# Performance work log

Measured on AMD Instinct MI355X. Metric: run time of the kernel, lower is better.

## Reference

```python
import jax, jax.numpy as jnp
import numpy as np

B, N, H = 4, 512, 64


def setup_inputs() -> dict:
    key = jax.random.key(0)
    ks = jax.random.split(key, 20)
    s = 0.05
    inp = {
        "positions": jax.random.uniform(ks[0], (B, N, 2), dtype=jnp.float32) * 10.0,
        "box_size": 10,
        # encoder: Linear(2,H) -> ReLU -> Linear(H,H)
        "enc_w1": jax.random.normal(ks[1], (2, H), jnp.float32) * s,
        "enc_b1": jnp.zeros((H,), jnp.float32),
        "enc_w2": jax.random.normal(ks[2], (H, H), jnp.float32) * s,
        "enc_b2": jnp.zeros((H,), jnp.float32),
        # message: Linear(2H+1,H) -> ReLU -> Linear(H,H)
        "msg_w1": jax.random.normal(ks[3], (2 * H + 1, H), jnp.float32) * s,
        "msg_b1": jnp.zeros((H,), jnp.float32),
        "msg_w2": jax.random.normal(ks[4], (H, H), jnp.float32) * s,
        "msg_b2": jnp.zeros((H,), jnp.float32),
        # update: Linear(2H,H) -> ReLU -> Linear(H,H)
        "upd_w1": jax.random.normal(ks[5], (2 * H, H), jnp.float32) * s,
        "upd_b1": jnp.zeros((H,), jnp.float32),
        "upd_w2": jax.random.normal(ks[6], (H, H), jnp.float32) * s,
        "upd_b2": jnp.zeros((H,), jnp.float32),
        # decoder: Linear(H,H) -> ReLU -> Linear(H,2)
        "dec_w1": jax.random.normal(ks[7], (H, H), jnp.float32) * s,
        "dec_b1": jnp.zeros((H,), jnp.float32),
        "dec_w2": jax.random.normal(ks[8], (H, 2), jnp.float32) * s,
        "dec_b2": jnp.zeros((2,), jnp.float32),
    }
    return inp


def reference(positions, box_size, enc_w1, enc_b1, enc_w2, enc_b2,
              msg_w1, msg_b1, msg_w2, msg_b2,
              upd_w1, upd_b1, upd_w2, upd_b2,
              dec_w1, dec_b1, dec_w2, dec_b2):
    box = jnp.float32(box_size)
    n = positions.shape[1]

    # encoder
    h = jax.nn.relu(positions @ enc_w1 + enc_b1) @ enc_w2 + enc_b2  # (B,N,H)

    # pairwise PBC displacement: r[b,i,j] = pos_j - pos_i (minimum image)
    r = positions[:, None, :, :] - positions[:, :, None, :]  # (B,N,N,2)
    r = r - box * jnp.round(r / box)
    dist = jnp.linalg.norm(r, axis=-1, keepdims=True)  # (B,N,N,1)

    # message MLP layer 1 without materializing concat: split msg_w1 rows
    w_i, w_j, w_d = msg_w1[:h.shape[-1]], msg_w1[h.shape[-1]:2 * h.shape[-1]], msg_w1[2 * h.shape[-1]:]
    a_i = h @ w_i  # (B,N,H) depends only on receiver i
    a_j = h @ w_j  # (B,N,H) depends only on sender j
    pre = a_i[:, :, None, :] + a_j[:, None, :, :] + dist * w_d[0] + msg_b1  # (B,N,N,H)
    m = jax.nn.relu(pre) @ msg_w2 + msg_b2  # (B,N,N,H)

    # mean over j != i
    mask = (1.0 - jnp.eye(n, dtype=m.dtype))[None, :, :, None]
    agg = jnp.sum(m * mask, axis=2) / jnp.float32(n - 1)  # (B,N,H)

    u_in = jnp.concatenate([h, agg], axis=-1)  # (B,N,2H)
    u = jax.nn.relu(u_in @ upd_w1 + upd_b1) @ upd_w2 + upd_b2
    forces = jax.nn.relu(u @ dec_w1 + dec_b1) @ dec_w2 + dec_b2  # (B,N,2)
    return forces
```

## Files before the change

kernel.cpp:

```cpp
#include <hip/hip_runtime.h>

#define BB 4
#define NN 512
#define HH 64
#define NODES (BB*NN)
#define SPLIT 8
#define JCH (NN/SPLIT)
#define TI 4

typedef float v4f __attribute__((ext_vector_type(4)));

__global__ __launch_bounds__(64) void enc_kernel(
    const float* __restrict__ pos,
    const float* __restrict__ enc_w1, const float* __restrict__ enc_b1,
    const float* __restrict__ enc_w2, const float* __restrict__ enc_b2,
    const float* __restrict__ msg_w1,
    float* __restrict__ h_out, float* __restrict__ ai_out, float* __restrict__ aj_out)
{
    const int node = blockIdx.x;
    const int k = threadIdx.x;
    __shared__ float t_s[HH];
    __shared__ float h_s[HH];

    const float px = pos[node*2+0];
    const float py = pos[node*2+1];

    float t = fmaf(px, enc_w1[k], fmaf(py, enc_w1[HH + k], enc_b1[k]));
    t_s[k] = fmaxf(t, 0.f);
    __syncthreads();

    float h = enc_b2[k];
    #pragma unroll
    for (int m = 0; m < HH; ++m) h = fmaf(t_s[m], enc_w2[m*HH + k], h);
    h_s[k] = h;
    h_out[node*HH + k] = h;
    __syncthreads();

    float ai = 0.f, aj = 0.f;
    #pragma unroll
    for (int m = 0; m < HH; ++m) {
        const float hm = h_s[m];
        ai = fmaf(hm, msg_w1[m*HH + k],        ai);
        aj = fmaf(hm, msg_w1[(HH + m)*HH + k], aj);
    }
    ai_out[node*HH + k] = ai;
    aj_out[node*HH + k] = aj;
}

__global__ __launch_bounds__(256) void pair_kernel(
    const float* __restrict__ pos, const int* __restrict__ box_ptr,
    const float* __restrict__ msg_w1, const float* __restrict__ msg_b1,
    const float* __restrict__ ai, const float* __restrict__ aj,
    float* __restrict__ acc_part)
{
    const int w  = threadIdx.x >> 6;
    const int l  = threadIdx.x & 63;
    const int jgrp = l >> 4;
    const int kq   = l & 15;
    const int wj = blockIdx.x*4 + w;
    const int s  = wj & (SPLIT-1);
    const int ig = wj >> 3;
    const int b  = ig >> 7;
    const int i0 = (ig & 127) * TI;
    const int jch0 = s * JCH;

    const float box  = (float)box_ptr[0];
    const float hbox = 0.5f * box;

    __shared__ float dbuf[4][TI*64];
    float* db = dbuf[w];

    const float2* pos2 = (const float2*)pos;

    const v4f wd4 = *(const v4f*)(msg_w1 + 2*HH*HH + 4*kq);
    const v4f b1  = *(const v4f*)(msg_b1 + 4*kq);
    v4f base4[TI];
    float2 pi[TI];
    #pragma unroll
    for (int ii = 0; ii < TI; ++ii) {
        const int node = b*NN + i0 + ii;
        base4[ii] = *(const v4f*)(ai + (size_t)node*HH + 4*kq) + b1;
        pi[ii] = pos2[node];
    }

    {
        const float2 pj = pos2[b*NN + jch0 + l];
        #pragma unroll
        for (int ii = 0; ii < TI; ++ii) {
            float dx = pj.x - pi[ii].x;
            float dy = pj.y - pi[ii].y;
            dx -= (dx >  hbox) ? box : 0.f;
            dx += (dx < -hbox) ? box : 0.f;
            dy -= (dy >  hbox) ? box : 0.f;
            dy += (dy < -hbox) ? box : 0.f;
            db[ii*64 + (l&3)*16 + (l>>2)] = sqrtf(fmaf(dx, dx, dy*dy));
        }
    }
    __builtin_amdgcn_wave_barrier();

    v4f acc[TI];
    #pragma unroll
    for (int ii = 0; ii < TI; ++ii) acc[ii] = (v4f){0.f,0.f,0.f,0.f};

    #pragma unroll
    for (int t4 = 0; t4 < 4; ++t4) {
        v4f d4[TI];
        #pragma unroll
        for (int ii = 0; ii < TI; ++ii)
            d4[ii] = *(const v4f*)(db + ii*64 + jgrp*16 + 4*t4);
        #pragma unroll
        for (int u = 0; u < 4; ++u) {
            const int o = (t4*4 + u)*4 + jgrp;
            const v4f a4 = *(const v4f*)(aj + (size_t)(b*NN + jch0 + o)*HH + 4*kq);
            #pragma unroll
            for (int ii = 0; ii < TI; ++ii) {
                const float d = d4[ii][u];
                v4f t = __builtin_elementwise_fma((v4f)(d), wd4, a4 + base4[ii]);
                acc[ii] += __builtin_elementwise_max(t, (v4f){0.f,0.f,0.f,0.f});
            }
        }
    }

    #pragma unroll
    for (int ii = 0; ii < TI; ++ii) {
        #pragma unroll
        for (int c = 0; c < 4; ++c) {
            float v = acc[ii][c];
            v += __shfl_xor(v, 16, 64);
            v += __shfl_xor(v, 32, 64);
            acc[ii][c] = v;
        }
    }

    {
        const int ii = jgrp;
        const int i  = i0 + ii;
        v4f a = acc[ii];
        if ((i >> 6) == s) {
            const v4f ajs = *(const v4f*)(aj + (size_t)(b*NN + i)*HH + 4*kq);
            v4f t = base4[ii] + ajs;
            a -= __builtin_elementwise_max(t, (v4f){0.f,0.f,0.f,0.f});
        }
        *(v4f*)(acc_part + ((size_t)s*NODES + b*NN + i)*HH + 4*kq) = a;
    }
}

__global__ __launch_bounds__(64) void out_kernel(
    const float* __restrict__ h_in, const float* __restrict__ acc_in,
    const float* __restrict__ msg_w2, const float* __restrict__ msg_b2,
    const float* __restrict__ upd_w1, const float* __restrict__ upd_b1,
    const float* __restrict__ upd_w2, const float* __restrict__ upd_b2,
    const float* __restrict__ dec_w1, const float* __restrict__ dec_b1,
    const float* __restrict__ dec_w2, const float* __restrict__ dec_b2,
    float* __restrict__ out)
{
    const int node = blockIdx.x;
    const int k = threadIdx.x;
    __shared__ float acc_s[HH], h_s[HH], agg_s[HH], p_s[HH], u_s[HH];

    float a = 0.f;
    #pragma unroll
    for (int sl = 0; sl < SPLIT; ++sl)
        a += acc_in[((size_t)sl*NODES + node)*HH + k];
    acc_s[k] = a;
    h_s[k]   = h_in[node*HH + k];
    __syncthreads();

    const float inv = 1.f / (float)(NN - 1);
    float agg = 0.f;
    #pragma unroll
    for (int m = 0; m < HH; ++m) agg = fmaf(acc_s[m], msg_w2[m*HH + k], agg);
    agg = fmaf(agg, inv, msg_b2[k]);
    agg_s[k] = agg;
    __syncthreads();

    float p = upd_b1[k];
    #pragma unroll
    for (int m = 0; m < HH; ++m) p = fmaf(h_s[m],   upd_w1[m*HH + k],        p);
    #pragma unroll
    for (int m = 0; m < HH; ++m) p = fmaf(agg_s[m], upd_w1[(HH + m)*HH + k], p);
    p_s[k] = fmaxf(p, 0.f);
    __syncthreads();

    float u = upd_b2[k];
    #pragma unroll
    for (int m = 0; m < HH; ++m) u = fmaf(p_s[m], upd_w2[m*HH + k], u);
    u_s[k] = u;
    __syncthreads();

    float d1 = dec_b1[k];
    #pragma unroll
    for (int m = 0; m < HH; ++m) d1 = fmaf(u_s[m], dec_w1[m*HH + k], d1);
    d1 = fmaxf(d1, 0.f);

    float f0 = d1 * dec_w2[k*2 + 0];
    float f1 = d1 * dec_w2[k*2 + 1];
    #pragma unroll
    for (int off = 32; off >= 1; off >>= 1) {
        f0 += __shfl_xor(f0, off, 64);
        f1 += __shfl_xor(f1, off, 64);
    }
    if (k == 0) {
        out[node*2 + 0] = f0 + dec_b2[0];
        out[node*2 + 1] = f1 + dec_b2[1];
    }
}

extern "C" void kernel_launch(void* const* d_in, const int* in_sizes, int n_in,
                              void* d_out, int out_size, void* d_ws, size_t ws_size,
                              hipStream_t stream) {
    const float* pos    = (const float*)d_in[0];
    const int*   boxp   = (const int*)  d_in[1];
    const float* enc_w1 = (const float*)d_in[2];
    const float* enc_b1 = (const float*)d_in[3];
    const float* enc_w2 = (const float*)d_in[4];
    const float* enc_b2 = (const float*)d_in[5];
    const float* msg_w1 = (const float*)d_in[6];
    const float* msg_b1 = (const float*)d_in[7];
    const float* msg_w2 = (const float*)d_in[8];
    const float* msg_b2 = (const float*)d_in[9];
    const float* upd_w1 = (const float*)d_in[10];
    const float* upd_b1 = (const float*)d_in[11];
    const float* upd_w2 = (const float*)d_in[12];
    const float* upd_b2 = (const float*)d_in[13];
    const float* dec_w1 = (const float*)d_in[14];
    const float* dec_b1 = (const float*)d_in[15];
    const float* dec_w2 = (const float*)d_in[16];
    const float* dec_b2 = (const float*)d_in[17];

    float* ws   = (float*)d_ws;
    float* h    = ws;
    float* ai   = ws + (size_t)NODES*HH;
    float* aj   = ws + (size_t)2*NODES*HH;
    float* accp = ws + (size_t)3*NODES*HH;

    enc_kernel<<<NODES, 64, 0, stream>>>(pos, enc_w1, enc_b1, enc_w2, enc_b2,
                                         msg_w1, h, ai, aj);
    pair_kernel<<<(NODES/TI)*SPLIT/4, 256, 0, stream>>>(pos, boxp, msg_w1, msg_b1,
                                                        ai, aj, accp);
    out_kernel<<<NODES, 64, 0, stream>>>(h, accp, msg_w2, msg_b2,
                                         upd_w1, upd_b1, upd_w2, upd_b2,
                                         dec_w1, dec_b1, dec_w2, dec_b2,
                                         (float*)d_out);
}
```

Baseline: 29.74 us.

## Fuse pair aggregation with node MLP epilogue and batch encoder nodes per block

The pair kernel and the output MLP kernel are merged into one kernel. Each 512-thread block handles 4 receiver nodes, with its 8 waves covering the 8 j-slices, and reduces the partial sums through LDS instead of a global workspace. Wave 0 then runs the msg_w2/update/decoder MLP chain for those 4 nodes, sharing each weight row across them with shuffles and LDS. The encoder also processes 4 nodes per 256-thread block. This removes a kernel launch and the global round trip of partial accumulators. In exchange, the serial epilogue runs on a single wave while the other 7 waves exit.

```diff
diff --git a/kernel.cpp b/kernel.cpp
--- a/kernel.cpp
+++ b/kernel.cpp
@@ -4,149 +4,55 @@
 #define NN 512
 #define HH 64
 #define NODES (BB*NN)
-#define SPLIT 8
-#define JCH (NN/SPLIT)
+#define NSL 8
+#define JCH (NN/NSL)
 #define TI 4
 
 typedef float v4f __attribute__((ext_vector_type(4)));
 
-__global__ __launch_bounds__(64) void enc_kernel(
+__global__ __launch_bounds__(256) void enc_kernel(
     const float* __restrict__ pos,
     const float* __restrict__ enc_w1, const float* __restrict__ enc_b1,
     const float* __restrict__ enc_w2, const float* __restrict__ enc_b2,
     const float* __restrict__ msg_w1,
     float* __restrict__ h_out, float* __restrict__ ai_out, float* __restrict__ aj_out)
 {
-    const int node = blockIdx.x;
-    const int k = threadIdx.x;
-    __shared__ float t_s[HH];
-    __shared__ float h_s[HH];
+    const int w = threadIdx.x >> 6;
+    const int k = threadIdx.x & 63;
+    const int node = blockIdx.x*4 + w;
+    __shared__ float t_s[4][HH];
+    __shared__ float h_s[4][HH];
 
     const float px = pos[node*2+0];
     const float py = pos[node*2+1];
 
     float t = fmaf(px, enc_w1[k], fmaf(py, enc_w1[HH + k], enc_b1[k]));
-    t_s[k] = fmaxf(t, 0.f);
+    t_s[w][k] = fmaxf(t, 0.f);
     __syncthreads();
 
     float h = enc_b2[k];
     #pragma unroll
-    for (int m = 0; m < HH; ++m) h = fmaf(t_s[m], enc_w2[m*HH + k], h);
-    h_s[k] = h;
+    for (int m = 0; m < HH; ++m) h = fmaf(t_s[w][m], enc_w2[m*HH + k], h);
+    h_s[w][k] = h;
     h_out[node*HH + k] = h;
     __syncthreads();
 
-    float ai = 0.f, aj = 0.f;
+    float aiv = 0.f, ajv = 0.f;
     #pragma unroll
     for (int m = 0; m < HH; ++m) {
-        const float hm = h_s[m];
-        ai = fmaf(hm, msg_w1[m*HH + k],        ai);
-        aj = fmaf(hm, msg_w1[(HH + m)*HH + k], aj);
-    }
-    ai_out[node*HH + k] = ai;
-    aj_out[node*HH + k] = aj;
+        const float hm = h_s[w][m];
+        aiv = fmaf(hm, msg_w1[m*HH + k],        aiv);
+        ajv = fmaf(hm, msg_w1[(HH + m)*HH + k], ajv);
+    }
+    ai_out[node*HH + k] = aiv;
+    aj_out[node*HH + k] = ajv;
 }
 
-__global__ __launch_bounds__(256) void pair_kernel(
+__global__ __launch_bounds__(512, 4) void pairout_kernel(
     const float* __restrict__ pos, const int* __restrict__ box_ptr,
     const float* __restrict__ msg_w1, const float* __restrict__ msg_b1,
     const float* __restrict__ ai, const float* __restrict__ aj,
-    float* __restrict__ acc_part)
-{
-    const int w  = threadIdx.x >> 6;
-    const int l  = threadIdx.x & 63;
-    const int jgrp = l >> 4;
-    const int kq   = l & 15;
-    const int wj = blockIdx.x*4 + w;
-    const int s  = wj & (SPLIT-1);
-    const int ig = wj >> 3;
-    const int b  = ig >> 7;
-    const int i0 = (ig & 127) * TI;
-    const int jch0 = s * JCH;
-
-    const float box  = (float)box_ptr[0];
-    const float hbox = 0.5f * box;
-
-    __shared__ float dbuf[4][TI*64];
-    float* db = dbuf[w];
-
-    const float2* pos2 = (const float2*)pos;
-
-    const v4f wd4 = *(const v4f*)(msg_w1 + 2*HH*HH + 4*kq);
-    const v4f b1  = *(const v4f*)(msg_b1 + 4*kq);
-    v4f base4[TI];
-    float2 pi[TI];
-    #pragma unroll
-    for (int ii = 0; ii < TI; ++ii) {
-        const int node = b*NN + i0 + ii;
-        base4[ii] = *(const v4f*)(ai + (size_t)node*HH + 4*kq) + b1;
-        pi[ii] = pos2[node];
-    }
-
-    {
-        const float2 pj = pos2[b*NN + jch0 + l];
-        #pragma unroll
-        for (int ii = 0; ii < TI; ++ii) {
-            float dx = pj.x - pi[ii].x;
-            float dy = pj.y - pi[ii].y;
-            dx -= (dx >  hbox) ? box : 0.f;
-            dx += (dx < -hbox) ? box : 0.f;
-            dy -= (dy >  hbox) ? box : 0.f;
-            dy += (dy < -hbox) ? box : 0.f;
-            db[ii*64 + (l&3)*16 + (l>>2)] = sqrtf(fmaf(dx, dx, dy*dy));
-        }
-    }
-    __builtin_amdgcn_wave_barrier();
-
-    v4f acc[TI];
-    #pragma unroll
-    for (int ii = 0; ii < TI; ++ii) acc[ii] = (v4f){0.f,0.f,0.f,0.f};
-
-    #pragma unroll
-    for (int t4 = 0; t4 < 4; ++t4) {
-        v4f d4[TI];
-        #pragma unroll
-        for (int ii = 0; ii < TI; ++ii)
-            d4[ii] = *(const v4f*)(db + ii*64 + jgrp*16 + 4*t4);
-        #pragma unroll
-        for (int u = 0; u < 4; ++u) {
-            const int o = (t4*4 + u)*4 + jgrp;
-            const v4f a4 = *(const v4f*)(aj + (size_t)(b*NN + jch0 + o)*HH + 4*kq);
-            #pragma unroll
-            for (int ii = 0; ii < TI; ++ii) {
-                const float d = d4[ii][u];
-                v4f t = __builtin_elementwise_fma((v4f)(d), wd4, a4 + base4[ii]);
-                acc[ii] += __builtin_elementwise_max(t, (v4f){0.f,0.f,0.f,0.f});
-            }
-        }
-    }
-
-    #pragma unroll
-    for (int ii = 0; ii < TI; ++ii) {
-        #pragma unroll
-        for (int c = 0; c < 4; ++c) {
-            float v = acc[ii][c];
-            v += __shfl_xor(v, 16, 64);
-            v += __shfl_xor(v, 32, 64);
-            acc[ii][c] = v;
-        }
-    }
-
-    {
-        const int ii = jgrp;
-        const int i  = i0 + ii;
-        v4f a = acc[ii];
-        if ((i >> 6) == s) {
-            const v4f ajs = *(const v4f*)(aj + (size_t)(b*NN + i)*HH + 4*kq);
-            v4f t = base4[ii] + ajs;
-            a -= __builtin_elementwise_max(t, (v4f){0.f,0.f,0.f,0.f});
-        }
-        *(v4f*)(acc_part + ((size_t)s*NODES + b*NN + i)*HH + 4*kq) = a;
-    }
-}
-
-__global__ __launch_bounds__(64) void out_kernel(
-    const float* __restrict__ h_in, const float* __restrict__ acc_in,
+    const float* __restrict__ h_in,
     const float* __restrict__ msg_w2, const float* __restrict__ msg_b2,
     const float* __restrict__ upd_w1, const float* __restrict__ upd_b1,
     const float* __restrict__ upd_w2, const float* __restrict__ upd_b2,
@@ -154,55 +60,257 @@
     const float* __restrict__ dec_w2, const float* __restrict__ dec_b2,
     float* __restrict__ out)
 {
-    const int node = blockIdx.x;
-    const int k = threadIdx.x;
-    __shared__ float acc_s[HH], h_s[HH], agg_s[HH], p_s[HH], u_s[HH];
-
-    float a = 0.f;
+    const int w  = threadIdx.x >> 6;
+    const int l  = threadIdx.x & 63;
+    const int jgrp = l >> 4;
+    const int kq   = l & 15;
+    const int ig = blockIdx.x;
+    const int b  = ig >> 7;
+    const int i0 = (ig & 127) * TI;
+    const int node0 = b*NN + i0;
+    const int jch0  = w * JCH;
+
+    __shared__ float dbuf[NSL][TI*64];
+    __shared__ float acc_lds[NSL][TI][HH];
+    __shared__ float C1[TI][HH];
+    __shared__ float C2[TI][HH];
+
+    {
+        const float box  = (float)box_ptr[0];
+        const float hbox = 0.5f * box;
+        const float2* pos2 = (const float2*)pos;
+        float* db = dbuf[w];
+
+        const v4f wd4 = *(const v4f*)(msg_w1 + 2*HH*HH + 4*kq);
+        const v4f b1  = *(const v4f*)(msg_b1 + 4*kq);
+        v4f base4[TI];
+        float2 pi[TI];
+        #pragma unroll
+        for (int ii = 0; ii < TI; ++ii) {
+            base4[ii] = *(const v4f*)(ai + (size_t)(node0 + ii)*HH + 4*kq) + b1;
+            pi[ii] = pos2[node0 + ii];
+        }
+
+        {
+            const float2 pj = pos2[b*NN + jch0 + l];
+            #pragma unroll
+            for (int ii = 0; ii < TI; ++ii) {
+                float dx = pj.x - pi[ii].x;
+                float dy = pj.y - pi[ii].y;
+                dx -= (dx >  hbox) ? box : 0.f;
+                dx += (dx < -hbox) ? box : 0.f;
+                dy -= (dy >  hbox) ? box : 0.f;
+                dy += (dy < -hbox) ? box : 0.f;
+                db[ii*64 + (l&3)*16 + (l>>2)] = sqrtf(fmaf(dx, dx, dy*dy));
+            }
+        }
+        __builtin_amdgcn_wave_barrier();
+
+        v4f acc[TI];
+        #pragma unroll
+        for (int ii = 0; ii < TI; ++ii) acc[ii] = (v4f){0.f,0.f,0.f,0.f};
+
+        #pragma unroll
+        for (int t4 = 0; t4 < 4; ++t4) {
+            v4f d4[TI];
+            #pragma unroll
+            for (int ii = 0; ii < TI; ++ii)
+                d4[ii] = *(const v4f*)(db + ii*64 + jgrp*16 + 4*t4);
+            #pragma unroll
+            for (int u = 0; u < 4; ++u) {
+                const int o = (t4*4 + u)*4 + jgrp;
+                const v4f a4 = *(const v4f*)(aj + (size_t)(b*NN + jch0 + o)*HH + 4*kq);
+                #pragma unroll
+                for (int ii = 0; ii < TI; ++ii) {
+                    const float d = d4[ii][u];
+                    v4f t = __builtin_elementwise_fma((v4f)(d), wd4, a4 + base4[ii]);
+                    acc[ii] += __builtin_elementwise_max(t, (v4f){0.f,0.f,0.f,0.f});
+                }
+            }
+        }
+
+        #pragma unroll
+        for (int ii = 0; ii < TI; ++ii) {
+            #pragma unroll
+            for (int c = 0; c < 4; ++c) {
+                float v = acc[ii][c];
+                v += __shfl_xor(v, 16, 64);
+                v += __shfl_xor(v, 32, 64);
+                acc[ii][c] = v;
+            }
+        }
+
+        {
+            const int ii = jgrp;
+            const int i  = i0 + ii;
+            v4f a = acc[ii];
+            if ((i >> 6) == w) {
+                const v4f ajs = *(const v4f*)(aj + (size_t)(b*NN + i)*HH + 4*kq);
+                a -= __builtin_elementwise_max(base4[ii] + ajs, (v4f){0.f,0.f,0.f,0.f});
+            }
+            *(v4f*)(&acc_lds[w][ii][4*kq]) = a;
+        }
+    }
+    __syncthreads();
+    if (w != 0) return;
+
+    float areg[TI], hreg[TI];
     #pragma unroll
-    for (int sl = 0; sl < SPLIT; ++sl)
-        a += acc_in[((size_t)sl*NODES + node)*HH + k];
-    acc_s[k] = a;
-    h_s[k]   = h_in[node*HH + k];
-    __syncthreads();
+    for (int nn = 0; nn < TI; ++nn) {
+        float a = 0.f;
+        #pragma unroll
+        for (int s = 0; s < NSL; ++s) a += acc_lds[s][nn][l];
+        areg[nn] = a;
+        hreg[nn] = h_in[(size_t)(node0 + nn)*HH + l];
+    }
 
     const float inv = 1.f / (float)(NN - 1);
-    float agg = 0.f;
-    #pragma unroll
-    for (int m = 0; m < HH; ++m) agg = fmaf(acc_s[m], msg_w2[m*HH + k], agg);
-    agg = fmaf(agg, inv, msg_b2[k]);
-    agg_s[k] = agg;
-    __syncthreads();
-
-    float p = upd_b1[k];
-    #pragma unroll
-    for (int m = 0; m < HH; ++m) p = fmaf(h_s[m],   upd_w1[m*HH + k],        p);
-    #pragma unroll
-    for (int m = 0; m < HH; ++m) p = fmaf(agg_s[m], upd_w1[(HH + m)*HH + k], p);
-    p_s[k] = fmaxf(p, 0.f);
-    __syncthreads();
-
-    float u = upd_b2[k];
-    #pragma unroll
-    for (int m = 0; m < HH; ++m) u = fmaf(p_s[m], upd_w2[m*HH + k], u);
-    u_s[k] = u;
-    __syncthreads();
-
-    float d1 = dec_b1[k];
-    #pragma unroll
-    for (int m = 0; m < HH; ++m) d1 = fmaf(u_s[m], dec_w1[m*HH + k], d1);
-    d1 = fmaxf(d1, 0.f);
-
-    float f0 = d1 * dec_w2[k*2 + 0];
-    float f1 = d1 * dec_w2[k*2 + 1];
-    #pragma unroll
-    for (int off = 32; off >= 1; off >>= 1) {
-        f0 += __shfl_xor(f0, off, 64);
-        f1 += __shfl_xor(f1, off, 64);
-    }
-    if (k == 0) {
-        out[node*2 + 0] = f0 + dec_b2[0];
-        out[node*2 + 1] = f1 + dec_b2[1];
+
+    {
+        v4f q[TI];
+        #pragma unroll
+        for (int nn = 0; nn < TI; ++nn) q[nn] = (v4f){0.f,0.f,0.f,0.f};
+        #pragma unroll
+        for (int mm = 0; mm < 16; ++mm) {
+            const int m = 4*mm + jgrp;
+            const v4f wrow = *(const v4f*)(msg_w2 + m*HH + 4*kq);
+            #pragma unroll
+            for (int nn = 0; nn < TI; ++nn) {
+                const float am = __shfl(areg[nn], m, 64);
+                q[nn] = __builtin_elementwise_fma((v4f)(am), wrow, q[nn]);
+            }
+        }
+        const v4f b2q = *(const v4f*)(msg_b2 + 4*kq);
+        #pragma unroll
+        for (int nn = 0; nn < TI; ++nn) {
+            v4f v = q[nn];
+            #pragma unroll
+            for (int c = 0; c < 4; ++c) {
+                float x = v[c];
+                x += __shfl_xor(x, 16, 64);
+                x += __shfl_xor(x, 32, 64);
+                v[c] = x;
+            }
+            v = __builtin_elementwise_fma(v, (v4f)(inv), b2q);
+            if (jgrp == 0) *(v4f*)(&C1[nn][4*kq]) = v;
+        }
+        __builtin_amdgcn_wave_barrier();
+    }
+
+    {
+        v4f q[TI];
+        #pragma unroll
+        for (int nn = 0; nn < TI; ++nn) q[nn] = (v4f){0.f,0.f,0.f,0.f};
+        #pragma unroll
+        for (int mm = 0; mm < 16; ++mm) {
+            const int m = 4*mm + jgrp;
+            const v4f wrow = *(const v4f*)(upd_w1 + m*HH + 4*kq);
+            #pragma unroll
+            for (int nn = 0; nn < TI; ++nn) {
+                const float hm = __shfl(hreg[nn], m, 64);
+                q[nn] = __builtin_elementwise_fma((v4f)(hm), wrow, q[nn]);
+            }
+        }
+        #pragma unroll
+        for (int mm = 0; mm < 16; ++mm) {
+            const int m = 4*mm + jgrp;
+            const v4f wrow = *(const v4f*)(upd_w1 + (size_t)(HH + m)*HH + 4*kq);
+            #pragma unroll
+            for (int nn = 0; nn < TI; ++nn) {
+                const float gm = C1[nn][m];
+                q[nn] = __builtin_elementwise_fma((v4f)(gm), wrow, q[nn]);
+            }
+        }
+        const v4f b1q = *(const v4f*)(upd_b1 + 4*kq);
+        #pragma unroll
+        for (int nn = 0; nn < TI; ++nn) {
+            v4f v = q[nn];
+            #pragma unroll
+            for (int c = 0; c < 4; ++c) {
+                float x = v[c];
+                x += __shfl_xor(x, 16, 64);
+                x += __shfl_xor(x, 32, 64);
+                v[c] = x;
+            }
+            v = __builtin_elementwise_max(v + b1q, (v4f){0.f,0.f,0.f,0.f});
+            if (jgrp == 0) *(v4f*)(&C2[nn][4*kq]) = v;
+        }
+        __builtin_amdgcn_wave_barrier();
+    }
+
+    {
+        v4f q[TI];
+        #pragma unroll
+        for (int nn = 0; nn < TI; ++nn) q[nn] = (v4f){0.f,0.f,0.f,0.f};
+        #pragma unroll
+        for (int mm = 0; mm < 16; ++mm) {
+            const int m = 4*mm + jgrp;
+            const v4f wrow = *(const v4f*)(upd_w2 + m*HH + 4*kq);
+            #pragma unroll
+            for (int nn = 0; nn < TI; ++nn) {
+                const float pm = C2[nn][m];
+                q[nn] = __builtin_elementwise_fma((v4f)(pm), wrow, q[nn]);
+            }
+        }
+        const v4f b2q = *(const v4f*)(upd_b2 + 4*kq);
+        #pragma unroll
+        for (int nn = 0; nn < TI; ++nn) {
+            v4f v = q[nn];
+            #pragma unroll
+            for (int c = 0; c < 4; ++c) {
+                float x = v[c];
+                x += __shfl_xor(x, 16, 64);
+                x += __shfl_xor(x, 32, 64);
+                v[c] = x;
+            }
+            v = v + b2q;
+            if (jgrp == 0) *(v4f*)(&C1[nn][4*kq]) = v;
+        }
+        __builtin_amdgcn_wave_barrier();
+    }
+
+    {
+        v4f q[TI];
+        #pragma unroll
+        for (int nn = 0; nn < TI; ++nn) q[nn] = (v4f){0.f,0.f,0.f,0.f};
+        #pragma unroll
+        for (int mm = 0; mm < 16; ++mm) {
+            const int m = 4*mm + jgrp;
+            const v4f wrow = *(const v4f*)(dec_w1 + m*HH + 4*kq);
+            #pragma unroll
+            for (int nn = 0; nn < TI; ++nn) {
+                const float um = C1[nn][m];
+                q[nn] = __builtin_elementwise_fma((v4f)(um), wrow, q[nn]);
+            }
+        }
+        const v4f db1q = *(const v4f*)(dec_b1 + 4*kq);
+        const v4f w2a  = *(const v4f*)(dec_w2 + 8*kq);
+        const v4f w2b  = *(const v4f*)(dec_w2 + 8*kq + 4);
+        const float fb0 = dec_b2[0];
+        const float fb1 = dec_b2[1];
+        #pragma unroll
+        for (int nn = 0; nn < TI; ++nn) {
+            v4f v = q[nn];
+            #pragma unroll
+            for (int c = 0; c < 4; ++c) {
+                float x = v[c];
+                x += __shfl_xor(x, 16, 64);
+                x += __shfl_xor(x, 32, 64);
+                v[c] = x;
+            }
+            v = __builtin_elementwise_max(v + db1q, (v4f){0.f,0.f,0.f,0.f});
+            float f0 = v[0]*w2a[0] + v[1]*w2a[2] + v[2]*w2b[0] + v[3]*w2b[2];
+            float f1 = v[0]*w2a[1] + v[1]*w2a[3] + v[2]*w2b[1] + v[3]*w2b[3];
+            #pragma unroll
+            for (int off = 1; off <= 8; off <<= 1) {
+                f0 += __shfl_xor(f0, off, 64);
+                f1 += __shfl_xor(f1, off, 64);
+            }
+            if (l == 0) {
+                out[(size_t)(node0 + nn)*2 + 0] = f0 + fb0;
+                out[(size_t)(node0 + nn)*2 + 1] = f1 + fb1;
+            }
+        }
     }
 }
 
@@ -228,18 +336,17 @@
     const float* dec_w2 = (const float*)d_in[16];
     const float* dec_b2 = (const float*)d_in[17];
 
-    float* ws   = (float*)d_ws;
-    float* h    = ws;
-    float* ai   = ws + (size_t)NODES*HH;
-    float* aj   = ws + (size_t)2*NODES*HH;
-    float* accp = ws + (size_t)3*NODES*HH;
-
-    enc_kernel<<<NODES, 64, 0, stream>>>(pos, enc_w1, enc_b1, enc_w2, enc_b2,
-                                         msg_w1, h, ai, aj);
-    pair_kernel<<<(NODES/TI)*SPLIT/4, 256, 0, stream>>>(pos, boxp, msg_w1, msg_b1,
-                                                        ai, aj, accp);
-    out_kernel<<<NODES, 64, 0, stream>>>(h, accp, msg_w2, msg_b2,
-                                         upd_w1, upd_b1, upd_w2, upd_b2,
-                                         dec_w1, dec_b1, dec_w2, dec_b2,
-                                         (float*)d_out);
+    float* ws = (float*)d_ws;
+    float* h  = ws;
+    float* ai = ws + (size_t)NODES*HH;
+    float* aj = ws + (size_t)2*NODES*HH;
+
+    enc_kernel<<<NODES/4, 256, 0, stream>>>(pos, enc_w1, enc_b1, enc_w2, enc_b2,
+                                            msg_w1, h, ai, aj);
+    pairout_kernel<<<NODES/TI, 512, 0, stream>>>(pos, boxp, msg_w1, msg_b1,
+                                                 ai, aj, h,
+                                                 msg_w2, msg_b2,
+                                                 upd_w1, upd_b1, upd_w2, upd_b2,
+                                                 dec_w1, dec_b1, dec_w2, dec_b2,
+                                                 (float*)d_out);
 }
```

After: 62.17 us. 2.09x slower.
